# Kernel optimization log

Measured on AMD Instinct MI355X. Metric: run time of the kernel, lower is better.

Reference implementation:

```python
import jax, jax.numpy as jnp
import numpy as np

TEMPERATURE = 0.07  # from init_kwargs
B, N, D = 256, 200000, 128


def setup_inputs() -> dict:
    key = jax.random.key(0)
    k1, k2, k3, k4, k5 = jax.random.split(key, 5)
    codes = jax.random.normal(k1, (B, D), dtype=jnp.float32)
    # Memory bank holds L2-normalized codes (update_memory stores normalized data)
    bank = jax.random.normal(k2, (N, D), dtype=jnp.float32)
    bank = bank / jnp.linalg.norm(bank, axis=1, keepdims=True)
    # background neighbours: ~51 nearest neighbours per sample (sparse mask)
    mask_bg = jax.random.uniform(k3, (B, N)) < (51.0 / N)
    # close-grouper cluster mates: ~N/number_of_centroids members per cluster
    mask_close = jax.random.uniform(k4, (B, N)) < (N / 100 / N)
    # guarantee self index present in both (include_self_index=True semantics)
    self_idx = jax.random.randint(k5, (B,), 0, N)
    rows = jnp.arange(B)
    mask_bg = mask_bg.at[rows, self_idx].set(True)
    mask_int = (mask_bg & mask_close).at[rows, self_idx].set(True)
    return {"codes": codes, "bank": bank, "mask_bg": mask_bg, "mask_int": mask_int}


def reference(codes, bank, mask_bg, mask_int):
    # v = F.normalize(codes, p=2, dim=1)
    v = codes / jnp.linalg.norm(codes, axis=1, keepdims=True)  # [B, D]
    # _prob_density: masked gather from bank, dot with code, exp(./T), sum.
    # Dense-equivalent: full dot matrix once, masked reductions for d1 and d2.
    dots = jnp.einsum("bd,nd->bn", v, bank) / TEMPERATURE  # [B, N]
    e = jnp.exp(dots)
    d1 = jnp.sum(jnp.where(mask_bg, e, 0.0), axis=1)   # background density
    d2 = jnp.sum(jnp.where(mask_int, e, 0.0), axis=1)  # intersect density
    loss = jnp.sum(jnp.log(d1) - jnp.log(d2)) / codes.shape[0]
    return loss
```

## Files before the change

kernel.cpp:

```cpp
#include <hip/hip_runtime.h>
#include <math.h>

#define BB 256
#define NN 200000
#define DD 128
#define INV_T 14.285714285714286f

#define CAPW 768
#define FLUSHW (CAPW - 512)

#define WS_VOTE  0
#define WS_SCALE 256
#define WS_P1    512
#define WS_P2    2560

__global__ __launch_bounds__(256) void la_init(const float* __restrict__ codes,
                                               const unsigned* __restrict__ mbg_w,
                                               unsigned* __restrict__ wsu) {
    __shared__ float s_red[4];
    __shared__ unsigned s_any[4];
    const int t = threadIdx.x;
    const unsigned lane = (unsigned)(t & 63);
    const unsigned wid = (unsigned)(t >> 6);
    const int b = blockIdx.x;

    const unsigned i = (unsigned)(b * 256 + t);
    const int any = (i < 50000u) && (mbg_w[i] > 1u);
    const unsigned long long bal = __ballot(any);
    if (lane == 0) s_any[wid] = (bal != 0ull) ? 1u : 0u;

    float c = (t < DD) ? codes[b * DD + t] : 0.f;
    float sq = c * c;
#pragma unroll
    for (int off = 32; off > 0; off >>= 1) sq += __shfl_down(sq, off, 64);
    if (lane == 0) s_red[wid] = sq;
    __syncthreads();
    if (t == 0) {
        float* wsf = (float*)wsu;
        wsf[WS_SCALE + b] = rsqrtf(s_red[0] + s_red[1] + s_red[2] + s_red[3]) * INV_T;
        wsu[WS_VOTE + b] = s_any[0] | s_any[1] | s_any[2] | s_any[3];
    }
}

__device__ __forceinline__ void process_wave(const float2* __restrict__ bank2,
                                             const unsigned* __restrict__ m32,
                                             const unsigned char* __restrict__ m8,
                                             const unsigned* __restrict__ ent,
                                             int cnt, int flag, int b,
                                             float2 cv, float scale,
                                             unsigned lane, float& l1, float& l2) {
    for (int i = 0; i < cnt; ++i) {
        const unsigned n = ent[i];
        const float2 bv = bank2[(size_t)n * 64u + lane];
        const unsigned im = (flag == 0) ? m32[(size_t)b * NN + n]
                                        : (unsigned)m8[(size_t)b * NN + n];
        float d = fmaf(cv.x, bv.x, cv.y * bv.y);
#pragma unroll
        for (int off = 32; off > 0; off >>= 1) d += __shfl_down(d, off, 64);
        if (lane == 0) {
            const float e = __expf(d * scale);
            l1 += e;
            if (im) l2 += e;
        }
    }
}

__global__ __launch_bounds__(256) void la_fused(const float* __restrict__ codes,
                                                const float* __restrict__ bank,
                                                const void* __restrict__ mbg_v,
                                                const void* __restrict__ mint_v,
                                                unsigned* __restrict__ wsu) {
    __shared__ unsigned s_ent[4][CAPW];
    __shared__ unsigned s_cnt[4];
    __shared__ float s_red[8];

    const int t = threadIdx.x;
    const unsigned lane = (unsigned)(t & 63);
    const unsigned wid = (unsigned)(t >> 6);
    const int s = blockIdx.x;
    const int b = blockIdx.y;

    const unsigned v4 = wsu[WS_VOTE + lane] | wsu[WS_VOTE + 64 + lane] |
                        wsu[WS_VOTE + 128 + lane] | wsu[WS_VOTE + 192 + lane];
    const int flag = (__ballot(v4 != 0u) != 0ull) ? 1 : 0;

    if (lane == 0) s_cnt[wid] = 0u;
    const float scale = ((const float*)wsu)[WS_SCALE + b];
    const float2 cv = ((const float2*)codes)[b * 64 + (int)lane];
    const float2* bank2 = (const float2*)bank;
    const unsigned* m32 = (const unsigned*)mint_v;
    const unsigned char* m8 = (const unsigned char*)mint_v;
    unsigned* ent = s_ent[wid];
    const int n_base = s * 25000;

    float l1 = 0.f, l2 = 0.f;

    if (flag == 0) {
        const uint4* row = (const uint4*)((const char*)mbg_v + (size_t)b * ((size_t)NN * 4)) + s * 6250;
        for (int it = 0; it < 13; ++it) {
            const int i0 = it * 512 + t;
            const int i1 = i0 + 256;
            uint4 v0 = make_uint4(0u, 0u, 0u, 0u), v1 = make_uint4(0u, 0u, 0u, 0u);
            if (i0 < 6250) v0 = row[i0];
            if (i1 < 6250) v1 = row[i1];
            const bool h0 = (v0.x | v0.y | v0.z | v0.w) != 0u;
            const bool h1 = (v1.x | v1.y | v1.z | v1.w) != 0u;
            if (__any((int)(h0 | h1))) {
                if (h0) {
                    const unsigned gw[4] = {v0.x, v0.y, v0.z, v0.w};
#pragma unroll
                    for (int j = 0; j < 4; ++j)
                        if (gw[j] != 0u) {
                            const unsigned pos = atomicAdd(&s_cnt[wid], 1u);
                            if (pos < CAPW) ent[pos] = (unsigned)(n_base + i0 * 4 + j);
                        }
                }
                if (h1) {
                    const unsigned gw[4] = {v1.x, v1.y, v1.z, v1.w};
#pragma unroll
                    for (int j = 0; j < 4; ++j)
                        if (gw[j] != 0u) {
                            const unsigned pos = atomicAdd(&s_cnt[wid], 1u);
                            if (pos < CAPW) ent[pos] = (unsigned)(n_base + i1 * 4 + j);
                        }
                }
                const int cnt = (int)*(volatile unsigned*)&s_cnt[wid];
                if (cnt >= FLUSHW) {
                    process_wave(bank2, m32, m8, ent, cnt, flag, b, cv, scale, lane, l1, l2);
                    if (lane == 0) s_cnt[wid] = 0u;
                }
            }
        }
    } else {
        const uint2* row2 = (const uint2*)((const char*)mbg_v + (size_t)b * NN) + s * 3125;
        for (int it = 0; it < 13; ++it) {
            const int i0 = it * 256 + t;
            uint2 v = make_uint2(0u, 0u);
            if (i0 < 3125) v = row2[i0];
            const bool h = (v.x | v.y) != 0u;
            if (__any((int)h)) {
                if (h) {
                    const unsigned gw[2] = {v.x, v.y};
#pragma unroll
                    for (int j = 0; j < 8; ++j)
                        if (((gw[j >> 2] >> ((j & 3) * 8)) & 0xffu) != 0u) {
                            const unsigned pos = atomicAdd(&s_cnt[wid], 1u);
                            if (pos < CAPW) ent[pos] = (unsigned)(n_base + i0 * 8 + j);
                        }
                }
                const int cnt = (int)*(volatile unsigned*)&s_cnt[wid];
                if (cnt >= FLUSHW) {
                    process_wave(bank2, m32, m8, ent, cnt, flag, b, cv, scale, lane, l1, l2);
                    if (lane == 0) s_cnt[wid] = 0u;
                }
            }
        }
    }

    int cnt = (int)*(volatile unsigned*)&s_cnt[wid];
    if (cnt > CAPW) cnt = CAPW;
    process_wave(bank2, m32, m8, ent, cnt, flag, b, cv, scale, lane, l1, l2);

    if (lane == 0) { s_red[wid] = l1; s_red[4 + wid] = l2; }
    __syncthreads();
    if (t == 0) {
        float* wsf = (float*)wsu;
        wsf[WS_P1 + b * 8 + s] = s_red[0] + s_red[1] + s_red[2] + s_red[3];
        wsf[WS_P2 + b * 8 + s] = s_red[4] + s_red[5] + s_red[6] + s_red[7];
    }
}

__global__ __launch_bounds__(256) void la_final(const unsigned* __restrict__ wsu,
                                                float* __restrict__ out) {
    __shared__ float red[4];
    const int t = threadIdx.x;
    const float* wsf = (const float*)wsu;
    float s1 = 0.f, s2 = 0.f;
#pragma unroll
    for (int s = 0; s < 8; ++s) {
        s1 += wsf[WS_P1 + t * 8 + s];
        s2 += wsf[WS_P2 + t * 8 + s];
    }
    float v = logf(s1) - logf(s2);
#pragma unroll
    for (int off = 32; off > 0; off >>= 1) v += __shfl_down(v, off, 64);
    if ((t & 63) == 0) red[t >> 6] = v;
    __syncthreads();
    if (t == 0) out[0] = (red[0] + red[1] + red[2] + red[3]) / (float)BB;
}

extern "C" void kernel_launch(void* const* d_in, const int* in_sizes, int n_in,
                              void* d_out, int out_size, void* d_ws, size_t ws_size,
                              hipStream_t stream) {
    const float* codes = (const float*)d_in[0];
    const float* bank  = (const float*)d_in[1];
    const void*  mbg   = d_in[2];
    const void*  mit   = d_in[3];

    unsigned* wsu = (unsigned*)d_ws;

    la_init<<<BB, 256, 0, stream>>>(codes, (const unsigned*)mbg, wsu);
    la_fused<<<dim3(8, BB), 256, 0, stream>>>(codes, bank, mbg, mit, wsu);
    la_final<<<1, 256, 0, stream>>>(wsu, (float*)d_out);
}
```

Before: 408.7 us.

## Fuse final reduction via last-block atomics and prefetch uint4 mask loads

Removes the separate final-reduction kernel by accumulating per-row densities with float atomics and letting the last finishing block compute the loss. In the byte-mask path it switches to 16-byte loads with software prefetch of the next chunk, so memory latency overlaps compaction. This saves one launch and may improve the mask-scan bandwidth. In exchange it adds atomics, a global done counter and nondeterministic float summation order.

```diff
diff --git a/kernel.cpp b/kernel.cpp
--- a/kernel.cpp
+++ b/kernel.cpp
@@ -11,8 +11,9 @@
 
 #define WS_VOTE  0
 #define WS_SCALE 256
-#define WS_P1    512
-#define WS_P2    2560
+#define WS_D1    512
+#define WS_D2    768
+#define WS_DONE  1024
 
 __global__ __launch_bounds__(256) void la_init(const float* __restrict__ codes,
                                                const unsigned* __restrict__ mbg_w,
@@ -39,6 +40,9 @@
         float* wsf = (float*)wsu;
         wsf[WS_SCALE + b] = rsqrtf(s_red[0] + s_red[1] + s_red[2] + s_red[3]) * INV_T;
         wsu[WS_VOTE + b] = s_any[0] | s_any[1] | s_any[2] | s_any[3];
+        wsf[WS_D1 + b] = 0.f;
+        wsf[WS_D2 + b] = 0.f;
+        if (b == 0) wsu[WS_DONE] = 0u;
     }
 }
 
@@ -69,10 +73,12 @@
                                                 const float* __restrict__ bank,
                                                 const void* __restrict__ mbg_v,
                                                 const void* __restrict__ mint_v,
-                                                unsigned* __restrict__ wsu) {
+                                                unsigned* __restrict__ wsu,
+                                                float* __restrict__ out) {
     __shared__ unsigned s_ent[4][CAPW];
     __shared__ unsigned s_cnt[4];
     __shared__ float s_red[8];
+    __shared__ int s_last;
 
     const int t = threadIdx.x;
     const unsigned lane = (unsigned)(t & 63);
@@ -132,28 +138,55 @@
             }
         }
     } else {
-        const uint2* row2 = (const uint2*)((const char*)mbg_v + (size_t)b * NN) + s * 3125;
-        for (int it = 0; it < 13; ++it) {
-            const int i0 = it * 256 + t;
-            uint2 v = make_uint2(0u, 0u);
-            if (i0 < 3125) v = row2[i0];
-            const bool h = (v.x | v.y) != 0u;
-            if (__any((int)h)) {
-                if (h) {
-                    const unsigned gw[2] = {v.x, v.y};
+        const uint4* row4 = (const uint4*)((const char*)mbg_v + (size_t)b * NN);
+        const int w0 = s * 1563;
+        const int wend = (s == 7) ? 12500 : (w0 + 1563);
+        uint4 cur = make_uint4(0u, 0u, 0u, 0u);
+        { const int i0 = w0 + t; if (i0 < wend) cur = row4[i0]; }
+        for (int it = 0; it < 7; ++it) {
+            uint4 nxt = make_uint4(0u, 0u, 0u, 0u);
+            if (it < 6) {
+                const int in = w0 + (it + 1) * 256 + t;
+                if (in < wend) nxt = row4[in];
+            }
+            const int ic = w0 + it * 256 + t;
+            const bool hl = (cur.x | cur.y) != 0u;
+            const bool hh = (cur.z | cur.w) != 0u;
+            if (__any((int)(hl | hh))) {
+                if (hl) {
+                    const unsigned gw[2] = {cur.x, cur.y};
 #pragma unroll
                     for (int j = 0; j < 8; ++j)
                         if (((gw[j >> 2] >> ((j & 3) * 8)) & 0xffu) != 0u) {
                             const unsigned pos = atomicAdd(&s_cnt[wid], 1u);
-                            if (pos < CAPW) ent[pos] = (unsigned)(n_base + i0 * 8 + j);
-                        }
-                }
-                const int cnt = (int)*(volatile unsigned*)&s_cnt[wid];
-                if (cnt >= FLUSHW) {
-                    process_wave(bank2, m32, m8, ent, cnt, flag, b, cv, scale, lane, l1, l2);
-                    if (lane == 0) s_cnt[wid] = 0u;
+                            if (pos < CAPW) ent[pos] = (unsigned)(ic * 16 + j);
+                        }
+                }
+                {
+                    const int cnt = (int)*(volatile unsigned*)&s_cnt[wid];
+                    if (cnt >= FLUSHW) {
+                        process_wave(bank2, m32, m8, ent, cnt, flag, b, cv, scale, lane, l1, l2);
+                        if (lane == 0) s_cnt[wid] = 0u;
+                    }
+                }
+                if (hh) {
+                    const unsigned gw[2] = {cur.z, cur.w};
+#pragma unroll
+                    for (int j = 0; j < 8; ++j)
+                        if (((gw[j >> 2] >> ((j & 3) * 8)) & 0xffu) != 0u) {
+                            const unsigned pos = atomicAdd(&s_cnt[wid], 1u);
+                            if (pos < CAPW) ent[pos] = (unsigned)(ic * 16 + 8 + j);
+                        }
+                }
+                {
+                    const int cnt = (int)*(volatile unsigned*)&s_cnt[wid];
+                    if (cnt >= FLUSHW) {
+                        process_wave(bank2, m32, m8, ent, cnt, flag, b, cv, scale, lane, l1, l2);
+                        if (lane == 0) s_cnt[wid] = 0u;
+                    }
                 }
             }
+            cur = nxt;
         }
     }
 
@@ -163,30 +196,26 @@
 
     if (lane == 0) { s_red[wid] = l1; s_red[4 + wid] = l2; }
     __syncthreads();
+    float* wsf = (float*)wsu;
     if (t == 0) {
-        float* wsf = (float*)wsu;
-        wsf[WS_P1 + b * 8 + s] = s_red[0] + s_red[1] + s_red[2] + s_red[3];
-        wsf[WS_P2 + b * 8 + s] = s_red[4] + s_red[5] + s_red[6] + s_red[7];
-    }
-}
-
-__global__ __launch_bounds__(256) void la_final(const unsigned* __restrict__ wsu,
-                                                float* __restrict__ out) {
-    __shared__ float red[4];
-    const int t = threadIdx.x;
-    const float* wsf = (const float*)wsu;
-    float s1 = 0.f, s2 = 0.f;
-#pragma unroll
-    for (int s = 0; s < 8; ++s) {
-        s1 += wsf[WS_P1 + t * 8 + s];
-        s2 += wsf[WS_P2 + t * 8 + s];
-    }
-    float v = logf(s1) - logf(s2);
-#pragma unroll
-    for (int off = 32; off > 0; off >>= 1) v += __shfl_down(v, off, 64);
-    if ((t & 63) == 0) red[t >> 6] = v;
+        atomicAdd(&wsf[WS_D1 + b], s_red[0] + s_red[1] + s_red[2] + s_red[3]);
+        atomicAdd(&wsf[WS_D2 + b], s_red[4] + s_red[5] + s_red[6] + s_red[7]);
+        __threadfence();
+        const unsigned old = atomicAdd(&wsu[WS_DONE], 1u);
+        s_last = (old == 8u * BB - 1u) ? 1 : 0;
+    }
     __syncthreads();
-    if (t == 0) out[0] = (red[0] + red[1] + red[2] + red[3]) / (float)BB;
+
+    if (s_last) {
+        const float d1v = atomicAdd(&wsf[WS_D1 + t], 0.f);
+        const float d2v = atomicAdd(&wsf[WS_D2 + t], 0.f);
+        float v = logf(d1v) - logf(d2v);
+#pragma unroll
+        for (int off = 32; off > 0; off >>= 1) v += __shfl_down(v, off, 64);
+        if (lane == 0) s_red[wid] = v;
+        __syncthreads();
+        if (t == 0) out[0] = (s_red[0] + s_red[1] + s_red[2] + s_red[3]) / (float)BB;
+    }
 }
 
 extern "C" void kernel_launch(void* const* d_in, const int* in_sizes, int n_in,
@@ -200,6 +229,5 @@
     unsigned* wsu = (unsigned*)d_ws;
 
     la_init<<<BB, 256, 0, stream>>>(codes, (const unsigned*)mbg, wsu);
-    la_fused<<<dim3(8, BB), 256, 0, stream>>>(codes, bank, mbg, mit, wsu);
-    la_final<<<1, 256, 0, stream>>>(wsu, (float*)d_out);
-}
+    la_fused<<<dim3(8, BB), 256, 0, stream>>>(codes, bank, mbg, mit, wsu, (float*)d_out);
+}
```

New measurement: 475.3 us. +16.3%, slower.
